# Optimization experiments

Hardware: AMD Instinct MI355X
Metric: run time of the kernel (lower is better)

## Reference

```python
import jax, jax.numpy as jnp
import numpy as np

B, H, W, C, F = 32, 32, 32, 256, 64
K_NEIGH = 32  # L1 pixel-distance cutoff used for the static mask


def _distance_mask(h, w, k):
    # coords: [hw, 2] of (y, x); L1 pixel distances, normalized by max(h, w)
    ys, xs = jnp.meshgrid(jnp.arange(h), jnp.arange(w), indexing='ij')
    coords = jnp.stack([ys, xs], axis=-1).reshape(-1, 2).astype(jnp.float32)
    diff = jnp.abs(coords[:, None, :] - coords[None, :, :]).sum(-1)  # [hw, hw], == cdist p=1
    dist = diff / float(max(h, w))
    return jnp.where(diff <= k, dist, 0.0)


def setup_inputs() -> dict:
    key = jax.random.key(0)
    ks = jax.random.split(key, 7)
    return {
        'feature_map': jax.random.normal(ks[0], (B, H, W, C), dtype=jnp.float32),
        'emb_W': jax.random.normal(ks[1], (F, C), dtype=jnp.float32) * (1.0 / np.sqrt(C)),
        'emb_b': jax.random.normal(ks[2], (F,), dtype=jnp.float32) * 0.01,
        'attn_W': jax.random.normal(ks[3], (C, C), dtype=jnp.float32) * (1.0 / np.sqrt(C)),
        'attn_b': jax.random.normal(ks[4], (C,), dtype=jnp.float32) * 0.01,
        'thr_W': jax.random.normal(ks[5], (1, C), dtype=jnp.float32) * (1.0 / np.sqrt(C)),
        'thr_b': jax.random.normal(ks[6], (1,), dtype=jnp.float32) * 0.01,
        'layer': 0,
    }


def reference(feature_map, emb_W, emb_b, attn_W, attn_b, thr_W, thr_b, layer):
    b, h, w, c = feature_map.shape
    hw = h * w
    x = feature_map.reshape(b, hw, c)  # row-major (y, x) flatten, matches torch view

    # 1x1 conv -> per-pixel linear: instance embeddings [b, hw, F]
    emb = jnp.einsum('bnc,fc->bnf', x, emb_W) + emb_b

    # squared Euclidean pairwise distances (cdist p=2, then squared)
    sq = jnp.sum(emb * emb, axis=-1)  # [b, hw]
    d2 = jnp.maximum(sq[:, :, None] + sq[:, None, :]
                     - 2.0 * jnp.einsum('bnf,bmf->bnm', emb, emb), 0.0)

    mask = _distance_mask(h, w, K_NEIGH)  # [hw, hw] static buffer
    sim = jax.nn.softmax(jnp.exp(-d2) - (1.0 - mask), axis=-1)  # [b, hw, hw]

    # shortcut = attention_conv(feature_map): [b, hw, c]
    shortcut = jnp.einsum('bnc,dc->bnd', x, attn_W) + attn_b

    # per-pixel learned threshold: [b, hw]
    Tinst = (jnp.einsum('bnc,oc->bno', shortcut, thr_W) + thr_b)[..., 0]

    A = jax.nn.softmax(jnp.maximum(sim - Tinst[:, None, :], 0.0), axis=-1)

    # bmm: out[b, i, c] = sum_j shortcut[b, j, c] * A[b, i, j]
    attn_out = jnp.einsum('bjc,bij->bic', shortcut, A)

    res = (x + attn_out).reshape(b, h, w, c)
    return res
```

## Files before the change

### kernel.cpp

```cpp
#include <hip/hip_runtime.h>
#include <hip/hip_bf16.h>


typedef short bf16x8 __attribute__((ext_vector_type(8)));
typedef float f32x4 __attribute__((ext_vector_type(4)));

__device__ __forceinline__ unsigned short f2bf(float f) {
  unsigned u = __float_as_uint(f);
  u += 0x7fffu + ((u >> 16) & 1u);
  return (unsigned short)(u >> 16);
}
__device__ __forceinline__ float bf2f(unsigned short h) {
  return __uint_as_float(((unsigned)h) << 16);
}
__device__ __forceinline__ unsigned pack2(float a, float b) {
  return (unsigned)f2bf(a) | ((unsigned)f2bf(b) << 16);
}
__device__ __forceinline__ f32x4 mfma16(bf16x8 a, bf16x8 b, f32x4 c) {
  return __builtin_amdgcn_mfma_f32_16x16x32_bf16(a, b, c, 0, 0, 0);
}
__device__ __forceinline__ int iabs(int v) { return v < 0 ? -v : v; }
__device__ __forceinline__ void load_lds16(const void* g, void* l) {
  __builtin_amdgcn_global_load_lds(
      (const __attribute__((address_space(1))) unsigned int*)g,
      (__attribute__((address_space(3))) unsigned int*)l, 16, 0, 0);
}

__global__ __launch_bounds__(256) void k_prep(const float* __restrict__ embW,
                                              const float* __restrict__ attnW,
                                              unsigned short* __restrict__ Wb) {
  const int i = (blockIdx.x * 256 + threadIdx.x) * 4;
  float4 v = (i < 16384) ? *(const float4*)(embW + i)
                         : *(const float4*)(attnW + (i - 16384));
  ushort4 p; p.x = f2bf(v.x); p.y = f2bf(v.y); p.z = f2bf(v.z); p.w = f2bf(v.w);
  *(ushort4*)(Wb + i) = p;
}

__global__ __launch_bounds__(256) void k_lin(const float* __restrict__ x,
                                             const unsigned short* __restrict__ Wb,
                                             const float* __restrict__ embB,
                                             const float* __restrict__ attnB,
                                             const float* __restrict__ thrW,
                                             const float* __restrict__ thrB,
                                             unsigned short* __restrict__ embb,
                                             float* __restrict__ sq,
                                             unsigned short* __restrict__ scT,
                                             float* __restrict__ Tout) {
  __shared__ union {
    struct { unsigned short xs[64][40]; unsigned short ws[320][40]; } a;
    unsigned short St[256][72];
  } sm;
  const int t = threadIdx.x;
  const int Mbase = blockIdx.x * 64;
  const int lane = t & 63, wave = t >> 6;
  const int wm = wave >> 1, wn = wave & 1;
  const int l15 = lane & 15, quad = lane >> 4;

  f32x4 acc[2][10] = {};
  for (int k0 = 0; k0 < 256; k0 += 32) {
    {
      int row = t >> 2, c0 = (t & 3) * 8;
      const float* src = x + (size_t)(Mbase + row) * 256 + k0 + c0;
      float4 a = *(const float4*)src;
      float4 b = *(const float4*)(src + 4);
      uint4 p; p.x = pack2(a.x, a.y); p.y = pack2(a.z, a.w);
      p.z = pack2(b.x, b.y); p.w = pack2(b.z, b.w);
      *(uint4*)&sm.a.xs[row][c0] = p;
    }
    {
      const unsigned short* wsrc = Wb + (size_t)t * 256 + k0;
      for (int s = 0; s < 4; s++)
        *(uint4*)&sm.a.ws[t][s * 8] = *(const uint4*)(wsrc + s * 8);
      if (t < 64) {
        const unsigned short* wsrc2 = Wb + (size_t)(256 + t) * 256 + k0;
        for (int s = 0; s < 4; s++)
          *(uint4*)&sm.a.ws[256 + t][s * 8] = *(const uint4*)(wsrc2 + s * 8);
      }
    }
    __syncthreads();
    bf16x8 af[2];
    af[0] = *(const bf16x8*)&sm.a.xs[wm * 32 + l15][quad * 8];
    af[1] = *(const bf16x8*)&sm.a.xs[wm * 32 + 16 + l15][quad * 8];
    for (int nt = 0; nt < 10; nt++) {
      bf16x8 bfr = *(const bf16x8*)&sm.a.ws[wn * 160 + nt * 16 + l15][quad * 8];
      acc[0][nt] = mfma16(af[0], bfr, acc[0][nt]);
      acc[1][nt] = mfma16(af[1], bfr, acc[1][nt]);
    }
    __syncthreads();
  }

  if (wn == 0) {
    float sp[2][4] = {{0.f,0.f,0.f,0.f},{0.f,0.f,0.f,0.f}};
    for (int rt = 0; rt < 2; rt++)
      for (int nt = 0; nt < 4; nt++) {
        int n = nt * 16 + l15;
        float bias = embB[n];
        for (int r = 0; r < 4; r++) {
          float v = acc[rt][nt][r] + bias;
          unsigned short hb = f2bf(v);
          int row = wm * 32 + rt * 16 + quad * 4 + r;
          embb[(size_t)(Mbase + row) * 64 + n] = hb;
          float vf = bf2f(hb);
          sp[rt][r] += vf * vf;
        }
      }
    for (int m = 8; m >= 1; m >>= 1)
      for (int rt = 0; rt < 2; rt++)
        for (int r = 0; r < 4; r++)
          sp[rt][r] += __shfl_xor(sp[rt][r], m);
    if (l15 == 0)
      for (int rt = 0; rt < 2; rt++)
        for (int r = 0; r < 4; r++)
          sq[Mbase + wm * 32 + rt * 16 + quad * 4 + r] = sp[rt][r];
  }

  for (int rt = 0; rt < 2; rt++)
    for (int nt = 0; nt < 10; nt++) {
      int n = wn * 160 + nt * 16 + l15;
      if (n < 64) continue;
      int c = n - 64;
      float bias = attnB[c];
      for (int r = 0; r < 4; r++) {
        float v = acc[rt][nt][r] + bias;
        sm.St[c][wm * 32 + rt * 16 + quad * 4 + r] = f2bf(v);
      }
    }
  __syncthreads();

  const int b = Mbase >> 10, jbase = Mbase & 1023;
  {
    unsigned short* dst = scT + ((size_t)b * 256 + t) * 1024 + jbase;
    for (int s = 0; s < 8; s++)
      *(uint4*)(dst + s * 8) = *(const uint4*)&sm.St[t][s * 8];
  }
  {
    float tp = 0.f;
    int j = t >> 2, cs = (t & 3) * 64;
    for (int c = 0; c < 64; c++)
      tp += bf2f(sm.St[cs + c][j]) * thrW[cs + c];
    tp += __shfl_xor(tp, 1);
    tp += __shfl_xor(tp, 2);
    if ((t & 3) == 0) Tout[Mbase + j] = tp + thrB[0];
  }
}

__global__ __launch_bounds__(512) void k_scores(const unsigned short* __restrict__ embb,
                                                const float* __restrict__ sq,
                                                const float* __restrict__ T,
                                                unsigned short* __restrict__ U,
                                                float* __restrict__ Z) {
  __shared__ unsigned short E_lds[16 * 1040];
  __shared__ float rbuf[16];
  __shared__ float mtab[64];
  const int t = threadIdx.x, lane = t & 63, wave = t >> 6;
  const int b = blockIdx.x >> 6, rb = (blockIdx.x & 63) * 16;
  const int l15 = lane & 15, quad = lane >> 4;
  const unsigned short* eb = embb + (size_t)b * 1024 * 64;

  if (t < 16) rbuf[t] = 0.f;
  if (t < 64) {
    float m = (t <= 32) ? (float)t * (1.f / 32.f) : 0.f;
    mtab[t] = __expf(m - 1.f);
  }
  __syncthreads();

  const int rowA = rb + l15;
  bf16x8 a0 = *(const bf16x8*)(eb + (size_t)rowA * 64 + quad * 8);
  bf16x8 a1 = *(const bf16x8*)(eb + (size_t)rowA * 64 + 32 + quad * 8);
  const int rloc = quad * 4;
  const int yi0 = (rb + rloc) >> 5, xi0 = (rb + rloc) & 31;
  float nsqi[4];
  for (int r = 0; r < 4; r++) nsqi[r] = -sq[b * 1024 + rb + rloc + r];
  const int jq = wave * 128;
  float rp[4] = {0.f, 0.f, 0.f, 0.f};
  for (int j0 = jq; j0 < jq + 128; j0 += 16) {
    const int jr = j0 + l15;
    bf16x8 b0 = *(const bf16x8*)(eb + (size_t)jr * 64 + quad * 8);
    bf16x8 b1 = *(const bf16x8*)(eb + (size_t)jr * 64 + 32 + quad * 8);
    f32x4 g = {0.f, 0.f, 0.f, 0.f};
    g = mfma16(a0, b0, g);
    g = mfma16(a1, b1, g);
    float sqj = sq[b * 1024 + jr];
    int dy = iabs(yi0 - (jr >> 5));
    int dxa = xi0 - (jr & 31);
    for (int r = 0; r < 4; r++) {
      float w = fminf(fmaf(2.f, g[r], nsqi[r] - sqj), 0.f);
      float v = __expf(w);
      int diff = dy + iabs(dxa + r);
      float e = __expf(v) * mtab[diff];
      E_lds[(rloc + r) * 1040 + jr] = f2bf(e);
      rp[r] += e;
    }
  }
  for (int m = 8; m >= 1; m >>= 1)
    for (int r = 0; r < 4; r++)
      rp[r] += __shfl_xor(rp[r], m);
  __syncthreads();
  if (l15 == 0)
    for (int r = 0; r < 4; r++)
      atomicAdd(&rbuf[rloc + r], rp[r]);
  __syncthreads();

  const int prow = t >> 5, seg = t & 31;
  const float invR = 1.f / rbuf[prow];
  const float* Tb = T + b * 1024;
  unsigned short* ur = U + ((size_t)(b * 1024 + rb + prow)) * 1024;
  float z = 0.f;
  for (int c = 0; c < 4; c++) {
    int j = c * 256 + seg * 8;
    union { bf16x8 v; unsigned short s[8]; } ev;
    ev.v = *(const bf16x8*)&E_lds[prow * 1040 + j];
    float4 t0 = *(const float4*)(Tb + j);
    float4 t1 = *(const float4*)(Tb + j + 4);
    float tf[8] = {t0.x, t0.y, t0.z, t0.w, t1.x, t1.y, t1.z, t1.w};
    union { uint4 v; unsigned short s[8]; } uo;
    for (int k = 0; k < 8; k++) {
      float u = __expf(fmaxf(fmaf(bf2f(ev.s[k]), invR, -tf[k]), 0.f));
      unsigned short h = f2bf(u);
      uo.s[k] = h;
      z += bf2f(h);
    }
    *(uint4*)(ur + j) = uo.v;
  }
  z += __shfl_xor(z, 1);
  z += __shfl_xor(z, 2);
  z += __shfl_xor(z, 4);
  z += __shfl_xor(z, 8);
  z += __shfl_xor(z, 16);
  if (seg == 0) Z[b * 1024 + rb + prow] = z;
}

__global__ __launch_bounds__(256) void k_out(const unsigned short* __restrict__ U,
                                             const float* __restrict__ Z,
                                             const unsigned short* __restrict__ scT,
                                             const float* __restrict__ x,
                                             float* __restrict__ out) {
  __shared__ unsigned short Ab[128 * 32];
  __shared__ unsigned short Bb[128 * 32];
  const int t = threadIdx.x, lane = t & 63, wave = t >> 6;
  const int wm = wave >> 1, wn = wave & 1;
  const int l15 = lane & 15, quad = lane >> 4;
  const int x8 = blockIdx.x & 7, s = blockIdx.x >> 3;
  const int b = x8 * 4 + (s >> 4), tile = s & 15;
  const int rb = (tile >> 1) * 128, cb = (tile & 1) * 128;

  const unsigned short* Ubase = U + (size_t)b * 1024 * 1024 + (size_t)rb * 1024;
  const unsigned short* Sbase = scT + (size_t)b * 256 * 1024 + (size_t)cb * 1024;

  int c0 = wave * 64 + lane;
  int c1 = c0 + 256;
  const int r0 = c0 >> 2, o0 = (c0 & 3) * 8;
  const int r1 = c1 >> 2, o1 = (c1 & 3) * 8;

  f32x4 acc[4][4] = {};
  for (int j0 = 0; j0 < 1024; j0 += 32) {
    load_lds16(Ubase + (size_t)r0 * 1024 + j0 + o0, Ab + c0 * 8);
    load_lds16(Ubase + (size_t)r1 * 1024 + j0 + o1, Ab + c1 * 8);
    load_lds16(Sbase + (size_t)r0 * 1024 + j0 + o0, Bb + c0 * 8);
    load_lds16(Sbase + (size_t)r1 * 1024 + j0 + o1, Bb + c1 * 8);
    __syncthreads();
    bf16x8 af[4], bf[4];
    for (int i = 0; i < 4; i++)
      af[i] = *(const bf16x8*)&Ab[(wm * 64 + i * 16 + l15) * 32 + quad * 8];
    for (int i = 0; i < 4; i++)
      bf[i] = *(const bf16x8*)&Bb[(wn * 64 + i * 16 + l15) * 32 + quad * 8];
    for (int i = 0; i < 4; i++)
      for (int j = 0; j < 4; j++)
        acc[i][j] = mfma16(af[i], bf[j], acc[i][j]);
    __syncthreads();
  }

  const int colb = cb + wn * 64;
  for (int i = 0; i < 4; i++) {
    int rowb = rb + wm * 64 + i * 16 + quad * 4;
    float iz[4];
    for (int r = 0; r < 4; r++) iz[r] = 1.f / Z[b * 1024 + rowb + r];
    for (int j = 0; j < 4; j++) {
      int c = colb + j * 16 + l15;
      for (int r = 0; r < 4; r++) {
        size_t idx = ((size_t)(b * 1024 + rowb + r)) * 256 + c;
        out[idx] = x[idx] + acc[i][j][r] * iz[r];
      }
    }
  }
}

extern "C" void kernel_launch(void* const* d_in, const int* in_sizes, int n_in,
                              void* d_out, int out_size, void* d_ws, size_t ws_size,
                              hipStream_t stream) {
  const float* x     = (const float*)d_in[0];
  const float* embW  = (const float*)d_in[1];
  const float* embB  = (const float*)d_in[2];
  const float* attnW = (const float*)d_in[3];
  const float* attnB = (const float*)d_in[4];
  const float* thrW  = (const float*)d_in[5];
  const float* thrB  = (const float*)d_in[6];
  float* out = (float*)d_out;

  char* ws = (char*)d_ws;
  unsigned short* embb = (unsigned short*)(ws);
  unsigned short* scT  = (unsigned short*)(ws + (4ull << 20));
  unsigned short* U    = (unsigned short*)(ws + (20ull << 20));
  unsigned short* Wb   = (unsigned short*)(ws + (36ull << 20));
  float* sq = (float*)(ws + (84ull << 20));
  float* T  = (float*)(ws + (84ull << 20) + (128ull << 10));
  float* Z  = (float*)(ws + (84ull << 20) + (256ull << 10));

  k_prep<<<80, 256, 0, stream>>>(embW, attnW, Wb);
  k_lin<<<512, 256, 0, stream>>>(x, Wb, embB, attnB, thrW, thrB, embb, sq, scT, T);
  k_scores<<<2048, 512, 0, stream>>>(embb, sq, T, U, Z);
  k_out<<<512, 256, 0, stream>>>(U, Z, scT, x, out);
}
```

Measured before the change: 193.3 us.

## Use base-2 exponentials, packed bf16 stores, transposed MFMA, double-buffered k_out

Prescales squared norms, thresholds and the mask table by log2(e) so the score kernel can use raw v_exp_f32 instead of __expf. It also swaps the MFMA operand order so each lane owns one row, and packs conversions with v_cvt_pk_bf16_f32. This lets it store E values as vectorized uint2 writes and reduce row sums with fewer shuffles. Separately, k_out double-buffers its LDS tiles so the global-to-LDS loads of the next K-slice overlap the MFMAs, at the cost of twice the LDS.

```diff
diff --git a/kernel.cpp b/kernel.cpp
--- a/kernel.cpp
+++ b/kernel.cpp
@@ -4,6 +4,8 @@
 
 typedef short bf16x8 __attribute__((ext_vector_type(8)));
 typedef float f32x4 __attribute__((ext_vector_type(4)));
+
+#define LOG2E 1.4426950408889634f
 
 __device__ __forceinline__ unsigned short f2bf(float f) {
   unsigned u = __float_as_uint(f);
@@ -15,6 +17,16 @@
 }
 __device__ __forceinline__ unsigned pack2(float a, float b) {
   return (unsigned)f2bf(a) | ((unsigned)f2bf(b) << 16);
+}
+__device__ __forceinline__ unsigned cvtpk(float lo, float hi) {
+  unsigned r;
+  asm("v_cvt_pk_bf16_f32 %0, %1, %2" : "=v"(r) : "v"(lo), "v"(hi));
+  return r;
+}
+__device__ __forceinline__ float exp2x(float x) {
+  float r;
+  asm("v_exp_f32 %0, %1" : "=v"(r) : "v"(x));
+  return r;
 }
 __device__ __forceinline__ f32x4 mfma16(bf16x8 a, bf16x8 b, f32x4 c) {
   return __builtin_amdgcn_mfma_f32_16x16x32_bf16(a, b, c, 0, 0, 0);
@@ -43,9 +55,9 @@
                                              const float* __restrict__ thrW,
                                              const float* __restrict__ thrB,
                                              unsigned short* __restrict__ embb,
-                                             float* __restrict__ sq,
+                                             float* __restrict__ sq2,
                                              unsigned short* __restrict__ scT,
-                                             float* __restrict__ Tout) {
+                                             float* __restrict__ T2out) {
   __shared__ union {
     struct { unsigned short xs[64][40]; unsigned short ws[320][40]; } a;
     unsigned short St[256][72];
@@ -111,7 +123,7 @@
     if (l15 == 0)
       for (int rt = 0; rt < 2; rt++)
         for (int r = 0; r < 4; r++)
-          sq[Mbase + wm * 32 + rt * 16 + quad * 4 + r] = sp[rt][r];
+          sq2[Mbase + wm * 32 + rt * 16 + quad * 4 + r] = sp[rt][r] * LOG2E;
   }
 
   for (int rt = 0; rt < 2; rt++)
@@ -140,87 +152,96 @@
       tp += bf2f(sm.St[cs + c][j]) * thrW[cs + c];
     tp += __shfl_xor(tp, 1);
     tp += __shfl_xor(tp, 2);
-    if ((t & 3) == 0) Tout[Mbase + j] = tp + thrB[0];
+    if ((t & 3) == 0) T2out[Mbase + j] = (tp + thrB[0]) * LOG2E;
   }
 }
 
 __global__ __launch_bounds__(512) void k_scores(const unsigned short* __restrict__ embb,
-                                                const float* __restrict__ sq,
-                                                const float* __restrict__ T,
+                                                const float* __restrict__ sq2,
+                                                const float* __restrict__ T2,
                                                 unsigned short* __restrict__ U,
                                                 float* __restrict__ Z) {
   __shared__ unsigned short E_lds[16 * 1040];
   __shared__ float rbuf[16];
-  __shared__ float mtab[64];
+  __shared__ float lm2[64];
   const int t = threadIdx.x, lane = t & 63, wave = t >> 6;
   const int b = blockIdx.x >> 6, rb = (blockIdx.x & 63) * 16;
   const int l15 = lane & 15, quad = lane >> 4;
   const unsigned short* eb = embb + (size_t)b * 1024 * 64;
+  const float* sq2b = sq2 + b * 1024;
 
   if (t < 16) rbuf[t] = 0.f;
   if (t < 64) {
     float m = (t <= 32) ? (float)t * (1.f / 32.f) : 0.f;
-    mtab[t] = __expf(m - 1.f);
-  }
-  __syncthreads();
-
-  const int rowA = rb + l15;
-  bf16x8 a0 = *(const bf16x8*)(eb + (size_t)rowA * 64 + quad * 8);
-  bf16x8 a1 = *(const bf16x8*)(eb + (size_t)rowA * 64 + 32 + quad * 8);
-  const int rloc = quad * 4;
-  const int yi0 = (rb + rloc) >> 5, xi0 = (rb + rloc) & 31;
-  float nsqi[4];
-  for (int r = 0; r < 4; r++) nsqi[r] = -sq[b * 1024 + rb + rloc + r];
+    lm2[t] = (m - 1.f) * LOG2E;
+  }
+  __syncthreads();
+
+  const int i = rb + l15;
+  bf16x8 if0 = *(const bf16x8*)(eb + (size_t)i * 64 + quad * 8);
+  bf16x8 if1 = *(const bf16x8*)(eb + (size_t)i * 64 + 32 + quad * 8);
+  const float nsq2i = -sq2b[i];
+  const int yi = i >> 5, xi = i & 31;
   const int jq = wave * 128;
-  float rp[4] = {0.f, 0.f, 0.f, 0.f};
+  float rp = 0.f;
+  #pragma unroll
   for (int j0 = jq; j0 < jq + 128; j0 += 16) {
     const int jr = j0 + l15;
-    bf16x8 b0 = *(const bf16x8*)(eb + (size_t)jr * 64 + quad * 8);
-    bf16x8 b1 = *(const bf16x8*)(eb + (size_t)jr * 64 + 32 + quad * 8);
+    bf16x8 jf0 = *(const bf16x8*)(eb + (size_t)jr * 64 + quad * 8);
+    bf16x8 jf1 = *(const bf16x8*)(eb + (size_t)jr * 64 + 32 + quad * 8);
     f32x4 g = {0.f, 0.f, 0.f, 0.f};
-    g = mfma16(a0, b0, g);
-    g = mfma16(a1, b1, g);
-    float sqj = sq[b * 1024 + jr];
-    int dy = iabs(yi0 - (jr >> 5));
-    int dxa = xi0 - (jr & 31);
-    for (int r = 0; r < 4; r++) {
-      float w = fminf(fmaf(2.f, g[r], nsqi[r] - sqj), 0.f);
-      float v = __expf(w);
-      int diff = dy + iabs(dxa + r);
-      float e = __expf(v) * mtab[diff];
-      E_lds[(rloc + r) * 1040 + jr] = f2bf(e);
-      rp[r] += e;
-    }
-  }
-  for (int m = 8; m >= 1; m >>= 1)
-    for (int r = 0; r < 4; r++)
-      rp[r] += __shfl_xor(rp[r], m);
-  __syncthreads();
-  if (l15 == 0)
-    for (int r = 0; r < 4; r++)
-      atomicAdd(&rbuf[rloc + r], rp[r]);
+    g = mfma16(jf0, if0, g);
+    g = mfma16(jf1, if1, g);
+    const int jg = j0 + quad * 4;
+    const float4 s4 = *(const float4*)(sq2b + jg);
+    const int dy = iabs(yi - (jg >> 5));
+    const int dxa = xi - (jg & 31);
+    float e0, e1, e2, e3;
+    {
+      float w2 = fminf(fmaf(2.f * LOG2E, g[0], nsq2i - s4.x), 0.f);
+      e0 = exp2x(fmaf(exp2x(w2), LOG2E, lm2[dy + iabs(dxa)]));
+      w2 = fminf(fmaf(2.f * LOG2E, g[1], nsq2i - s4.y), 0.f);
+      e1 = exp2x(fmaf(exp2x(w2), LOG2E, lm2[dy + iabs(dxa - 1)]));
+      w2 = fminf(fmaf(2.f * LOG2E, g[2], nsq2i - s4.z), 0.f);
+      e2 = exp2x(fmaf(exp2x(w2), LOG2E, lm2[dy + iabs(dxa - 2)]));
+      w2 = fminf(fmaf(2.f * LOG2E, g[3], nsq2i - s4.w), 0.f);
+      e3 = exp2x(fmaf(exp2x(w2), LOG2E, lm2[dy + iabs(dxa - 3)]));
+    }
+    rp += (e0 + e1) + (e2 + e3);
+    uint2 pk; pk.x = cvtpk(e0, e1); pk.y = cvtpk(e2, e3);
+    *(uint2*)&E_lds[l15 * 1040 + jg] = pk;
+  }
+  rp += __shfl_xor(rp, 16);
+  rp += __shfl_xor(rp, 32);
+  __syncthreads();
+  if (quad == 0) atomicAdd(&rbuf[l15], rp);
   __syncthreads();
 
   const int prow = t >> 5, seg = t & 31;
-  const float invR = 1.f / rbuf[prow];
-  const float* Tb = T + b * 1024;
+  const float invR2 = LOG2E / rbuf[prow];
+  const float* T2b = T2 + b * 1024;
   unsigned short* ur = U + ((size_t)(b * 1024 + rb + prow)) * 1024;
   float z = 0.f;
+  #pragma unroll
   for (int c = 0; c < 4; c++) {
     int j = c * 256 + seg * 8;
     union { bf16x8 v; unsigned short s[8]; } ev;
     ev.v = *(const bf16x8*)&E_lds[prow * 1040 + j];
-    float4 t0 = *(const float4*)(Tb + j);
-    float4 t1 = *(const float4*)(Tb + j + 4);
+    float4 t0 = *(const float4*)(T2b + j);
+    float4 t1 = *(const float4*)(T2b + j + 4);
     float tf[8] = {t0.x, t0.y, t0.z, t0.w, t1.x, t1.y, t1.z, t1.w};
-    union { uint4 v; unsigned short s[8]; } uo;
-    for (int k = 0; k < 8; k++) {
-      float u = __expf(fmaxf(fmaf(bf2f(ev.s[k]), invR, -tf[k]), 0.f));
-      unsigned short h = f2bf(u);
-      uo.s[k] = h;
-      z += bf2f(h);
-    }
-    *(uint4*)(ur + j) = uo.v;
+    uint4 uo;
+    unsigned q[4];
+    #pragma unroll
+    for (int h = 0; h < 4; h++) {
+      float u0 = exp2x(fmaxf(fmaf(bf2f(ev.s[2 * h]), invR2, -tf[2 * h]), 0.f));
+      float u1 = exp2x(fmaxf(fmaf(bf2f(ev.s[2 * h + 1]), invR2, -tf[2 * h + 1]), 0.f));
+      unsigned qq = cvtpk(u0, u1);
+      q[h] = qq;
+      z += __uint_as_float(qq << 16) + __uint_as_float(qq & 0xffff0000u);
+    }
+    uo.x = q[0]; uo.y = q[1]; uo.z = q[2]; uo.w = q[3];
+    *(uint4*)(ur + j) = uo;
   }
   z += __shfl_xor(z, 1);
   z += __shfl_xor(z, 2);
@@ -235,8 +256,8 @@
                                              const unsigned short* __restrict__ scT,
                                              const float* __restrict__ x,
                                              float* __restrict__ out) {
-  __shared__ unsigned short Ab[128 * 32];
-  __shared__ unsigned short Bb[128 * 32];
+  __shared__ unsigned short Ab[2][128 * 32];
+  __shared__ unsigned short Bb[2][128 * 32];
   const int t = threadIdx.x, lane = t & 63, wave = t >> 6;
   const int wm = wave >> 1, wn = wave & 1;
   const int l15 = lane & 15, quad = lane >> 4;
@@ -247,28 +268,43 @@
   const unsigned short* Ubase = U + (size_t)b * 1024 * 1024 + (size_t)rb * 1024;
   const unsigned short* Sbase = scT + (size_t)b * 256 * 1024 + (size_t)cb * 1024;
 
-  int c0 = wave * 64 + lane;
-  int c1 = c0 + 256;
+  const int c0 = wave * 64 + lane;
+  const int c1 = c0 + 256;
   const int r0 = c0 >> 2, o0 = (c0 & 3) * 8;
   const int r1 = c1 >> 2, o1 = (c1 & 3) * 8;
+  const unsigned short* ua0 = Ubase + (size_t)r0 * 1024 + o0;
+  const unsigned short* ua1 = Ubase + (size_t)r1 * 1024 + o1;
+  const unsigned short* sa0 = Sbase + (size_t)r0 * 1024 + o0;
+  const unsigned short* sa1 = Sbase + (size_t)r1 * 1024 + o1;
+
+#define STAGE(bufi, j0)                              \
+  do {                                               \
+    load_lds16(ua0 + (j0), &Ab[bufi][c0 * 8]);       \
+    load_lds16(ua1 + (j0), &Ab[bufi][c1 * 8]);       \
+    load_lds16(sa0 + (j0), &Bb[bufi][c0 * 8]);       \
+    load_lds16(sa1 + (j0), &Bb[bufi][c1 * 8]);       \
+  } while (0)
 
   f32x4 acc[4][4] = {};
-  for (int j0 = 0; j0 < 1024; j0 += 32) {
-    load_lds16(Ubase + (size_t)r0 * 1024 + j0 + o0, Ab + c0 * 8);
-    load_lds16(Ubase + (size_t)r1 * 1024 + j0 + o1, Ab + c1 * 8);
-    load_lds16(Sbase + (size_t)r0 * 1024 + j0 + o0, Bb + c0 * 8);
-    load_lds16(Sbase + (size_t)r1 * 1024 + j0 + o1, Bb + c1 * 8);
-    __syncthreads();
-    bf16x8 af[4], bf[4];
+  STAGE(0, 0);
+  __syncthreads();
+  int cur = 0;
+  for (int it = 0; it < 32; ++it) {
+    if (it < 31) STAGE(cur ^ 1, (it + 1) * 32);
+    bf16x8 af[4], bfr[4];
     for (int i = 0; i < 4; i++)
-      af[i] = *(const bf16x8*)&Ab[(wm * 64 + i * 16 + l15) * 32 + quad * 8];
+      af[i] = *(const bf16x8*)&Ab[cur][(wm * 64 + i * 16 + l15) * 32 + quad * 8];
     for (int i = 0; i < 4; i++)
-      bf[i] = *(const bf16x8*)&Bb[(wn * 64 + i * 16 + l15) * 32 + quad * 8];
+      bfr[i] = *(const bf16x8*)&Bb[cur][(wn * 64 + i * 16 + l15) * 32 + quad * 8];
     for (int i = 0; i < 4; i++)
       for (int j = 0; j < 4; j++)
-        acc[i][j] = mfma16(af[i], bf[j], acc[i][j]);
-    __syncthreads();
-  }
+        acc[i][j] = mfma16(af[i], bfr[j], acc[i][j]);
+    if (it < 31) {
+      __syncthreads();
+      cur ^= 1;
+    }
+  }
+#undef STAGE
 
   const int colb = cb + wn * 64;
   for (int i = 0; i < 4; i++) {
@@ -302,12 +338,12 @@
   unsigned short* scT  = (unsigned short*)(ws + (4ull << 20));
   unsigned short* U    = (unsigned short*)(ws + (20ull << 20));
   unsigned short* Wb   = (unsigned short*)(ws + (36ull << 20));
-  float* sq = (float*)(ws + (84ull << 20));
-  float* T  = (float*)(ws + (84ull << 20) + (128ull << 10));
-  float* Z  = (float*)(ws + (84ull << 20) + (256ull << 10));
+  float* sq2 = (float*)(ws + (84ull << 20));
+  float* T2  = (float*)(ws + (84ull << 20) + (128ull << 10));
+  float* Z   = (float*)(ws + (84ull << 20) + (256ull << 10));
 
   k_prep<<<80, 256, 0, stream>>>(embW, attnW, Wb);
-  k_lin<<<512, 256, 0, stream>>>(x, Wb, embB, attnB, thrW, thrB, embb, sq, scT, T);
-  k_scores<<<2048, 512, 0, stream>>>(embb, sq, T, U, Z);
+  k_lin<<<512, 256, 0, stream>>>(x, Wb, embB, attnB, thrW, thrB, embb, sq2, scT, T2);
+  k_scores<<<2048, 512, 0, stream>>>(embb, sq2, T2, U, Z);
   k_out<<<512, 256, 0, stream>>>(U, Z, scT, x, out);
 }
```

Measured after the change: 197.7 us. 2.3% more time.
